# Kernel optimization log

Measured on AMD Instinct MI355X. Metric: run time of the kernel, lower is better.

The kernel has to match this reference:

```python
import jax, jax.numpy as jnp
import numpy as np

ALPHA = 0.5
BETA = 5.0
LOGIT_SCALE = 100.0  # exp(log(100)) -- CLIP's learned logit scale at its clamp value
NUM_CLASSES = 200


def _l2norm(x):
    return x / jnp.linalg.norm(x, axis=-1, keepdims=True)


def setup_inputs() -> dict:
    key = jax.random.key(0)
    k1, k2, k3, k4 = jax.random.split(key, 4)
    img_f = jax.random.normal(k1, (1024, 512), dtype=jnp.float32)
    text_features = jax.random.normal(k2, (200, 512), dtype=jnp.float32)
    keys = jax.random.normal(k3, (50000, 512), dtype=jnp.float32)
    labels = jax.random.randint(k4, (50000,), 0, NUM_CLASSES, dtype=jnp.int64)
    return {"img_f": img_f, "text_features": text_features, "keys": keys, "labels": labels}


def reference(img_f, text_features, keys, labels):
    # encode_image output is L2-normalized in the module; keys were built from
    # normalized image features, text_features are normalized class embeddings.
    q = _l2norm(img_f)            # [B, D]
    t = _l2norm(text_features)    # [C, D]
    k = _l2norm(keys)             # [N, D]

    # CLIP zero-shot branch: scale * q @ t.T -> [B, C]
    z = LOGIT_SCALE * jnp.einsum('bd,cd->bc', q, t)

    # Tip-Adapter cache branch: exp(beta * q @ keys.T) @ one_hot(labels)
    sim = jnp.einsum('bd,nd->bn', q, k)                 # [B, N]
    aff = jnp.exp(BETA * sim)                           # [B, N]
    values = jax.nn.one_hot(labels, NUM_CLASSES, dtype=aff.dtype)  # [N, C]
    c = aff @ values                                    # [B, C]

    return (1.0 - ALPHA) * z + ALPHA * c
```

## Files before the change

kernel.cpp:

```cpp
#include <hip/hip_runtime.h>

#define B_Q    1024
#define D_K    512
#define N_CLS  200
#define N_KEYS 50000
#define N_PAD  50048
#define N_EXT  (N_PAD + 256)
#define N_ZT   (N_PAD / 128)

typedef __attribute__((ext_vector_type(8))) short bf16x8;
typedef __attribute__((ext_vector_type(4))) float f32x4;

__device__ __forceinline__ unsigned short f2bf(float f) {
  union { float f; unsigned int i; } v; v.f = f;
  unsigned int r = v.i + 0x7fffu + ((v.i >> 16) & 1u);
  return (unsigned short)(r >> 16);
}
__device__ __forceinline__ uint4 pack8(const float f[8], float s) {
  uint4 o;
  o.x = (unsigned)f2bf(f[0]*s) | ((unsigned)f2bf(f[1]*s) << 16);
  o.y = (unsigned)f2bf(f[2]*s) | ((unsigned)f2bf(f[3]*s) << 16);
  o.z = (unsigned)f2bf(f[4]*s) | ((unsigned)f2bf(f[5]*s) << 16);
  o.w = (unsigned)f2bf(f[6]*s) | ((unsigned)f2bf(f[7]*s) << 16);
  return o;
}
__device__ __forceinline__ void async_copy16(const void* g, void* lds) {
  __builtin_amdgcn_global_load_lds(
      (const __attribute__((address_space(1))) unsigned int*)g,
      (__attribute__((address_space(3))) unsigned int*)lds, 16, 0, 0);
}

__global__ void k_histscan(const int* __restrict__ labels, int* __restrict__ hist,
                           int* __restrict__ cursor) {
  __shared__ int h[N_CLS];
  __shared__ int lastFlag;
  int t = threadIdx.x;
  if (t < N_CLS) h[t] = 0;
  __syncthreads();
  int n = blockIdx.x * 256 + t;
  if (n < N_KEYS) atomicAdd(&h[labels[n]], 1);
  __syncthreads();
  if (t < N_CLS && h[t]) atomicAdd(&hist[t], h[t]);
  __threadfence();
  if (t == 0) lastFlag = (atomicAdd(&hist[255], 1) == (int)gridDim.x - 1);
  __syncthreads();
  if (!lastFlag) return;
  __shared__ int s[N_CLS];
  int v = 0;
  if (t < N_CLS) { v = atomicAdd(&hist[t], 0); s[t] = v; }
  __syncthreads();
  for (int d = 1; d < N_CLS; d <<= 1) {
    int x = 0;
    if (t < N_CLS && t >= d) x = s[t - d];
    __syncthreads();
    if (t < N_CLS) s[t] += x;
    __syncthreads();
  }
  if (t < N_CLS) cursor[t] = s[t] - v;
}

__global__ void k_perm(const int* __restrict__ labels, int* __restrict__ cursor,
                       int* __restrict__ dest) {
  __shared__ int lh[N_CLS];
  __shared__ int lbase[N_CLS];
  int t = threadIdx.x;
  if (t < N_CLS) lh[t] = 0;
  __syncthreads();
  int n = blockIdx.x * 256 + t;
  bool valid = (n < N_KEYS);
  int l = 0, lo = 0;
  if (valid) { l = labels[n]; lo = atomicAdd(&lh[l], 1); }
  __syncthreads();
  if (t < N_CLS && lh[t] > 0) lbase[t] = atomicAdd(&cursor[t], lh[t]);
  __syncthreads();
  if (valid) dest[n] = lbase[l] + lo;
}

__global__ void k_prep2(const float* __restrict__ keys, const float* __restrict__ img,
                        const float* __restrict__ txt, const int* __restrict__ labels,
                        const int* __restrict__ dest, unsigned short* __restrict__ qn,
                        unsigned short* __restrict__ kn, int* __restrict__ cls) {
  int w = threadIdx.x >> 6, lane = threadIdx.x & 63;
  int row = blockIdx.x * 4 + w;
  const float* src; unsigned short* dst; int r;
  if (row < N_PAD) {
    if (row >= N_KEYS) {
      *((uint4*)(kn + (size_t)row * D_K) + lane) = make_uint4(0, 0, 0, 0);
      if (lane == 0) cls[row] = N_CLS;
      return;
    }
    int d = dest[row];
    if (lane == 0) cls[d] = labels[row];
    src = keys + (size_t)row * D_K;
    dst = kn + (size_t)d * D_K;
  } else if (row < N_PAD + B_Q) {
    r = row - N_PAD;
    src = img + (size_t)r * D_K;
    dst = qn + (size_t)r * D_K;
  } else if (row < N_PAD + B_Q + N_CLS) {
    r = row - N_PAD - B_Q;
    src = txt + (size_t)r * D_K;
    dst = kn + (size_t)(N_PAD + r) * D_K;
  } else if (row < N_PAD + B_Q + N_CLS + 56) {
    r = N_PAD + N_CLS + (row - N_PAD - B_Q - N_CLS);
    *((uint4*)(kn + (size_t)r * D_K) + lane) = make_uint4(0, 0, 0, 0);
    return;
  } else return;
  const float4* s4 = (const float4*)src + lane * 2;
  float4 a = s4[0], b = s4[1];
  float f[8] = {a.x, a.y, a.z, a.w, b.x, b.y, b.z, b.w};
  float ss = 0.f;
#pragma unroll
  for (int i = 0; i < 8; i++) ss += f[i] * f[i];
#pragma unroll
  for (int d = 1; d < 64; d <<= 1) ss += __shfl_xor(ss, d);
  float rinv = rsqrtf(ss);
  *((uint4*)dst + lane) = pack8(f, rinv);
}

__global__ __launch_bounds__(256, 3) void k_main(const unsigned short* __restrict__ qn,
                                                 const unsigned short* __restrict__ kn,
                                                 const int* __restrict__ cls,
                                                 float* __restrict__ out) {
  __shared__ unsigned short As[2][128 * 64];
  int t = threadIdx.x;
  int tileB = blockIdx.x, tileN = blockIdx.y;
  int rowB0 = tileB * 128, rowN0 = tileN * 128;

  f32x4 acc[4][4];
#pragma unroll
  for (int i = 0; i < 4; i++)
#pragma unroll
    for (int j = 0; j < 4; j++) acc[i][j] = (f32x4){0.f, 0.f, 0.f, 0.f};

  int lane = t & 63, w = t >> 6;
  int wr = (w >> 1) * 64, wc = (w & 1) * 64;
  int l15 = lane & 15, lq = lane >> 4;
  const int rA = t >> 3;
  const int gsw = ((t & 7) ^ (rA & 7)) * 8;
  const int sw = l15 & 7;

  const unsigned short* bptr[4];
#pragma unroll
  for (int j = 0; j < 4; j++)
    bptr[j] = kn + (size_t)(rowN0 + wc + 16 * j + l15) * D_K + lq * 8;

#pragma unroll
  for (int i = 0; i < 4; i++)
    async_copy16(qn + (size_t)(rowB0 + i * 32 + rA) * D_K + gsw, &As[0][i * 2048 + t * 8]);

  for (int kt = 0; kt < 8; kt++) {
    int cur = kt & 1;
    __syncthreads();
    if (kt < 7) {
      int k0n = (kt + 1) * 64;
#pragma unroll
      for (int i = 0; i < 4; i++)
        async_copy16(qn + (size_t)(rowB0 + i * 32 + rA) * D_K + k0n + gsw,
                     &As[cur ^ 1][i * 2048 + t * 8]);
    }
    int k0 = kt * 64;
#pragma unroll
    for (int ks = 0; ks < 64; ks += 32) {
      bf16x8 af[4], bf[4];
#pragma unroll
      for (int j = 0; j < 4; j++)
        bf[j] = *(const bf16x8*)(bptr[j] + k0 + ks);
#pragma unroll
      for (int i = 0; i < 4; i++)
        af[i] = *(const bf16x8*)&As[cur][(wr + 16 * i + l15) * 64 + ((((ks >> 3) + lq) ^ sw) * 8)];
#pragma unroll
      for (int i = 0; i < 4; i++)
#pragma unroll
        for (int j = 0; j < 4; j++)
          acc[i][j] = __builtin_amdgcn_mfma_f32_16x16x32_bf16(af[i], bf[j], acc[i][j], 0, 0, 0);
    }
  }

  if (tileN >= N_ZT) {
#pragma unroll
    for (int i = 0; i < 4; i++)
#pragma unroll
      for (int j = 0; j < 4; j++) {
        int col = rowN0 + wc + 16 * j + l15 - N_PAD;
        if (col < N_CLS) {
#pragma unroll
          for (int r = 0; r < 4; r++) {
            int row = rowB0 + wr + 16 * i + lq * 4 + r;
            atomicAdd(out + (size_t)row * N_CLS + col, 50.0f * acc[i][j][r]);
          }
        }
      }
    return;
  }

#pragma unroll
  for (int i = 0; i < 4; i++)
#pragma unroll
    for (int j = 0; j < 4; j++)
#pragma unroll
      for (int r = 0; r < 4; r++) acc[i][j][r] = __expf(5.0f * acc[i][j][r]);

  int cj[4];
#pragma unroll
  for (int j = 0; j < 4; j++) cj[j] = cls[rowN0 + wc + 16 * j + l15];
  int cseg0 = cls[rowN0 + wc];
  int cseg1 = cls[rowN0 + wc + 63];

  for (int c = cseg0; c <= cseg1; c++) {
    if (c >= N_CLS) break;
#pragma unroll
    for (int i = 0; i < 4; i++) {
      float s0 = 0.f, s1 = 0.f, s2 = 0.f, s3 = 0.f;
#pragma unroll
      for (int j = 0; j < 4; j++) {
        if (cj[j] == c) {
          s0 += acc[i][j][0]; s1 += acc[i][j][1];
          s2 += acc[i][j][2]; s3 += acc[i][j][3];
        }
      }
#pragma unroll
      for (int d = 1; d < 16; d <<= 1) {
        s0 += __shfl_xor(s0, d); s1 += __shfl_xor(s1, d);
        s2 += __shfl_xor(s2, d); s3 += __shfl_xor(s3, d);
      }
      if (l15 == 0) {
        int row = rowB0 + wr + 16 * i + lq * 4;
        float* o = out + (size_t)row * N_CLS + c;
        if (s0 != 0.f) atomicAdd(o + 0 * N_CLS, 0.5f * s0);
        if (s1 != 0.f) atomicAdd(o + 1 * N_CLS, 0.5f * s1);
        if (s2 != 0.f) atomicAdd(o + 2 * N_CLS, 0.5f * s2);
        if (s3 != 0.f) atomicAdd(o + 3 * N_CLS, 0.5f * s3);
      }
    }
  }
}

extern "C" void kernel_launch(void* const* d_in, const int* in_sizes, int n_in,
                              void* d_out, int out_size, void* d_ws, size_t ws_size,
                              hipStream_t stream) {
  (void)in_sizes; (void)n_in; (void)out_size; (void)ws_size;
  const float* img    = (const float*)d_in[0];
  const float* txt    = (const float*)d_in[1];
  const float* keys   = (const float*)d_in[2];
  const int*   labels = (const int*)d_in[3];
  float*       out    = (float*)d_out;

  char* ws = (char*)d_ws;
  unsigned short* qn = (unsigned short*)(ws + 0);
  unsigned short* kn = (unsigned short*)(ws + 1048576);
  int*  dest   = (int*)(ws + 52559872);
  int*  cls    = (int*)(ws + 52760064);
  int*  hist   = (int*)(ws + 52960256);
  int*  cursor = (int*)(ws + 52961280);

  hipMemsetAsync(hist, 0, 256 * sizeof(int), stream);
  hipMemsetAsync(out, 0, (size_t)B_Q * N_CLS * sizeof(float), stream);

  k_histscan<<<196, 256, 0, stream>>>(labels, hist, cursor);
  k_perm<<<196, 256, 0, stream>>>(labels, cursor, dest);
  k_prep2<<<(N_PAD + B_Q + N_CLS + 56 + 3) / 4, 256, 0, stream>>>(
      keys, img, txt, labels, dest, qn, kn, cls);
  k_main<<<dim3(B_Q / 128, N_ZT + 2), 256, 0, stream>>>(qn, kn, cls, out);
}
```

Before: 314.6 us.

## Stage B tiles through LDS with register prefetch and fold output zeroing into prep

The main GEMM kernel used to read the keys (B operand) straight from global memory with per-lane vector loads. It now stages both A and B tiles through LDS, using register-held prefetch of the next k-slice and a single LDS buffer per operand in place of async global-to-LDS double buffering. The output memset is removed and its zeroing is folded into the prep kernel, and cls entries for the text and pad rows are now written explicitly. This is meant to improve B reuse and coalescing and to save one memset launch. The cost is an extra barrier per k-step and higher register pressure from the prefetch registers.

Result: slower. 395.2 us (+25.6%).

```diff
diff --git a/kernel.cpp b/kernel.cpp
--- a/kernel.cpp
+++ b/kernel.cpp
@@ -5,8 +5,13 @@
 #define N_CLS  200
 #define N_KEYS 50000
 #define N_PAD  50048
-#define N_EXT  (N_PAD + 256)
 #define N_ZT   (N_PAD / 128)
+
+#define R0 N_PAD
+#define R1 (R0 + B_Q)
+#define R2 (R1 + N_CLS)
+#define R3 (R2 + 56)
+#define R4 (R3 + 400)
 
 typedef __attribute__((ext_vector_type(8))) short bf16x8;
 typedef __attribute__((ext_vector_type(4))) float f32x4;
@@ -24,11 +29,6 @@
   o.w = (unsigned)f2bf(f[6]*s) | ((unsigned)f2bf(f[7]*s) << 16);
   return o;
 }
-__device__ __forceinline__ void async_copy16(const void* g, void* lds) {
-  __builtin_amdgcn_global_load_lds(
-      (const __attribute__((address_space(1))) unsigned int*)g,
-      (__attribute__((address_space(3))) unsigned int*)lds, 16, 0, 0);
-}
 
 __global__ void k_histscan(const int* __restrict__ labels, int* __restrict__ hist,
                            int* __restrict__ cursor) {
@@ -79,11 +79,12 @@
 __global__ void k_prep2(const float* __restrict__ keys, const float* __restrict__ img,
                         const float* __restrict__ txt, const int* __restrict__ labels,
                         const int* __restrict__ dest, unsigned short* __restrict__ qn,
-                        unsigned short* __restrict__ kn, int* __restrict__ cls) {
+                        unsigned short* __restrict__ kn, int* __restrict__ cls,
+                        float* __restrict__ out) {
   int w = threadIdx.x >> 6, lane = threadIdx.x & 63;
   int row = blockIdx.x * 4 + w;
-  const float* src; unsigned short* dst; int r;
-  if (row < N_PAD) {
+  const float* src; unsigned short* dst;
+  if (row < R0) {
     if (row >= N_KEYS) {
       *((uint4*)(kn + (size_t)row * D_K) + lane) = make_uint4(0, 0, 0, 0);
       if (lane == 0) cls[row] = N_CLS;
@@ -93,17 +94,25 @@
     if (lane == 0) cls[d] = labels[row];
     src = keys + (size_t)row * D_K;
     dst = kn + (size_t)d * D_K;
-  } else if (row < N_PAD + B_Q) {
-    r = row - N_PAD;
+  } else if (row < R1) {
+    int r = row - R0;
     src = img + (size_t)r * D_K;
     dst = qn + (size_t)r * D_K;
-  } else if (row < N_PAD + B_Q + N_CLS) {
-    r = row - N_PAD - B_Q;
+  } else if (row < R2) {
+    int r = row - R1;
+    if (lane == 0) cls[N_PAD + r] = N_CLS;
     src = txt + (size_t)r * D_K;
     dst = kn + (size_t)(N_PAD + r) * D_K;
-  } else if (row < N_PAD + B_Q + N_CLS + 56) {
-    r = N_PAD + N_CLS + (row - N_PAD - B_Q - N_CLS);
+  } else if (row < R3) {
+    int r = N_PAD + N_CLS + (row - R2);
     *((uint4*)(kn + (size_t)r * D_K) + lane) = make_uint4(0, 0, 0, 0);
+    if (lane == 0) cls[r] = N_CLS;
+    return;
+  } else if (row < R4) {
+    int zr = row - R3;
+    uint4* o4 = (uint4*)(out + (size_t)zr * 512) + lane * 2;
+    o4[0] = make_uint4(0, 0, 0, 0);
+    o4[1] = make_uint4(0, 0, 0, 0);
     return;
   } else return;
   const float4* s4 = (const float4*)src + lane * 2;
@@ -122,7 +131,8 @@
                                                  const unsigned short* __restrict__ kn,
                                                  const int* __restrict__ cls,
                                                  float* __restrict__ out) {
-  __shared__ unsigned short As[2][128 * 64];
+  __shared__ unsigned short As[128 * 64];
+  __shared__ unsigned short Bs[128 * 64];
   int t = threadIdx.x;
   int tileB = blockIdx.x, tileN = blockIdx.y;
   int rowB0 = tileB * 128, rowN0 = tileN * 128;
@@ -140,40 +150,59 @@
   const int gsw = ((t & 7) ^ (rA & 7)) * 8;
   const int sw = l15 & 7;
 
-  const unsigned short* bptr[4];
-#pragma unroll
-  for (int j = 0; j < 4; j++)
-    bptr[j] = kn + (size_t)(rowN0 + wc + 16 * j + l15) * D_K + lq * 8;
-
-#pragma unroll
-  for (int i = 0; i < 4; i++)
-    async_copy16(qn + (size_t)(rowB0 + i * 32 + rA) * D_K + gsw, &As[0][i * 2048 + t * 8]);
+  const unsigned short* aq = qn + (size_t)(rowB0 + rA) * D_K + gsw;
+  const unsigned short* bk = kn + (size_t)(rowN0 + rA) * D_K + gsw;
+
+  int cj[4];
+#pragma unroll
+  for (int j = 0; j < 4; j++) cj[j] = cls[rowN0 + wc + 16 * j + l15];
+  int cseg0 = cls[rowN0 + wc];
+  int cseg1 = cls[rowN0 + wc + 63];
+
+  uint4 va[4], vb[4];
+#pragma unroll
+  for (int i = 0; i < 4; i++) {
+    va[i] = *(const uint4*)(aq + i * 32 * D_K);
+    vb[i] = *(const uint4*)(bk + i * 32 * D_K);
+  }
+#pragma unroll
+  for (int i = 0; i < 4; i++) {
+    *(uint4*)&As[i * 2048 + t * 8] = va[i];
+    *(uint4*)&Bs[i * 2048 + t * 8] = vb[i];
+  }
 
   for (int kt = 0; kt < 8; kt++) {
-    int cur = kt & 1;
-    __syncthreads();
     if (kt < 7) {
       int k0n = (kt + 1) * 64;
 #pragma unroll
-      for (int i = 0; i < 4; i++)
-        async_copy16(qn + (size_t)(rowB0 + i * 32 + rA) * D_K + k0n + gsw,
-                     &As[cur ^ 1][i * 2048 + t * 8]);
-    }
-    int k0 = kt * 64;
+      for (int i = 0; i < 4; i++) {
+        va[i] = *(const uint4*)(aq + i * 32 * D_K + k0n);
+        vb[i] = *(const uint4*)(bk + i * 32 * D_K + k0n);
+      }
+    }
+    __syncthreads();
 #pragma unroll
     for (int ks = 0; ks < 64; ks += 32) {
       bf16x8 af[4], bf[4];
 #pragma unroll
+      for (int i = 0; i < 4; i++)
+        af[i] = *(const bf16x8*)&As[(wr + 16 * i + l15) * 64 + ((((ks >> 3) + lq) ^ sw) * 8)];
+#pragma unroll
       for (int j = 0; j < 4; j++)
-        bf[j] = *(const bf16x8*)(bptr[j] + k0 + ks);
-#pragma unroll
-      for (int i = 0; i < 4; i++)
-        af[i] = *(const bf16x8*)&As[cur][(wr + 16 * i + l15) * 64 + ((((ks >> 3) + lq) ^ sw) * 8)];
+        bf[j] = *(const bf16x8*)&Bs[(wc + 16 * j + l15) * 64 + ((((ks >> 3) + lq) ^ sw) * 8)];
 #pragma unroll
       for (int i = 0; i < 4; i++)
 #pragma unroll
         for (int j = 0; j < 4; j++)
           acc[i][j] = __builtin_amdgcn_mfma_f32_16x16x32_bf16(af[i], bf[j], acc[i][j], 0, 0, 0);
+    }
+    if (kt < 7) {
+      __syncthreads();
+#pragma unroll
+      for (int i = 0; i < 4; i++) {
+        *(uint4*)&As[i * 2048 + t * 8] = va[i];
+        *(uint4*)&Bs[i * 2048 + t * 8] = vb[i];
+      }
     }
   }
 
@@ -200,12 +229,6 @@
     for (int j = 0; j < 4; j++)
 #pragma unroll
       for (int r = 0; r < 4; r++) acc[i][j][r] = __expf(5.0f * acc[i][j][r]);
-
-  int cj[4];
-#pragma unroll
-  for (int j = 0; j < 4; j++) cj[j] = cls[rowN0 + wc + 16 * j + l15];
-  int cseg0 = cls[rowN0 + wc];
-  int cseg1 = cls[rowN0 + wc + 63];
 
   for (int c = cseg0; c <= cseg1; c++) {
     if (c >= N_CLS) break;
@@ -251,15 +274,12 @@
   unsigned short* kn = (unsigned short*)(ws + 1048576);
   int*  dest   = (int*)(ws + 52559872);
   int*  cls    = (int*)(ws + 52760064);
-  int*  hist   = (int*)(ws + 52960256);
-  int*  cursor = (int*)(ws + 52961280);
+  int*  hist   = (int*)(ws + 52961280);
+  int*  cursor = (int*)(ws + 52962304);
 
   hipMemsetAsync(hist, 0, 256 * sizeof(int), stream);
-  hipMemsetAsync(out, 0, (size_t)B_Q * N_CLS * sizeof(float), stream);
-
   k_histscan<<<196, 256, 0, stream>>>(labels, hist, cursor);
   k_perm<<<196, 256, 0, stream>>>(labels, cursor, dest);
-  k_prep2<<<(N_PAD + B_Q + N_CLS + 56 + 3) / 4, 256, 0, stream>>>(
-      keys, img, txt, labels, dest, qn, kn, cls);
+  k_prep2<<<(R4 + 3) / 4, 256, 0, stream>>>(keys, img, txt, labels, dest, qn, kn, cls, out);
   k_main<<<dim3(B_Q / 128, N_ZT + 2), 256, 0, stream>>>(qn, kn, cls, out);
 }
```
